# Performance work log

Measured on AMD Instinct MI355X. Metric: run time of the kernel, lower is better.

The kernel has to match this reference:

```python
import jax, jax.numpy as jnp
import numpy as np

B, S, N, C, D = 1, 6, 10000, 128, 4
HEADS, PTS = 4, 8
HF, WF = 28, 50
M = HF * WF


def setup_inputs() -> dict:
    key0 = jax.random.key(0)
    ks = jax.random.split(key0, 14)
    sc = C ** -0.5
    d = {}
    d["query"] = jax.random.normal(ks[0], (B, N, C), jnp.float32)
    d["key"] = jax.random.normal(ks[1], (S, M, B, C), jnp.float32)
    d["value"] = jax.random.normal(ks[2], (S, M, B, C), jnp.float32)
    d["query_pos"] = jax.random.normal(ks[3], (B, N, C), jnp.float32) * 0.1
    d["reference_points_cam"] = jax.random.uniform(ks[4], (S, B, N, D, 2), jnp.float32, -0.2, 1.2)
    d["bev_mask"] = jax.random.randint(ks[5], (S, B, N, D), 0, 2).astype(bool)
    d["w_off"] = jax.random.normal(ks[6], (C, HEADS * PTS * 2), jnp.float32) * sc
    d["b_off"] = jax.random.normal(ks[7], (HEADS * PTS * 2,), jnp.float32) * 0.01
    d["w_attn"] = jax.random.normal(ks[8], (C, HEADS * PTS), jnp.float32) * sc
    d["b_attn"] = jax.random.normal(ks[9], (HEADS * PTS,), jnp.float32) * 0.01
    d["w_val"] = jax.random.normal(ks[10], (C, C), jnp.float32) * sc
    d["b_val"] = jax.random.normal(ks[11], (C,), jnp.float32) * 0.01
    d["w_out"] = jax.random.normal(ks[12], (C, C), jnp.float32) * sc
    d["b_out"] = jax.random.normal(ks[13], (C,), jnp.float32) * 0.01
    d["Hf"] = HF
    d["Wf"] = WF
    return d


def reference(query, key, value, query_pos, reference_points_cam, bev_mask,
              w_off, b_off, w_attn, b_attn, w_val, b_val, w_out, b_out, Hf, Wf):
    # SpatialCrossAttention with MSDeformAttn3D (BEVFormer semantics, eval mode: dropout=identity).
    # The torch data-dependent gather/rebatch/scatter is replaced by mathematically equivalent
    # masked computation: deformable attention is per-query independent, so running it for all
    # BEV queries per camera and mask-accumulating yields identical slots.
    B_, N_, C_ = query.shape
    S_ = key.shape[0]
    D_ = reference_points_cam.shape[3]
    H, P = HEADS, PTS
    dh = C_ // H
    Pd = P // D_
    q = query + query_pos  # (B,N,C)
    off = (q @ w_off + b_off).reshape(B_, N_, H, Pd, D_, 2)
    aw = jax.nn.softmax((q @ w_attn + b_attn).reshape(B_, N_, H, P), axis=-1)  # over levels*points (L=1)
    # value projection; per-camera feature maps laid out as (B,S,H,Hf*Wf,dh)
    v = jnp.transpose(value, (2, 0, 1, 3))  # (B,S,M,C)
    v = v @ w_val + b_val
    v = v.reshape(B_, S_, Hf * Wf, H, dh).transpose(0, 1, 3, 2, 4)  # (B,S,H,M,dh)
    ref = jnp.transpose(reference_points_cam, (1, 0, 2, 3, 4))  # (B,S,N,D,2)
    norm = jnp.array([Wf, Hf], jnp.float32)  # offset_normalizer = (W, H)
    loc = ref[:, :, :, None, None, :, :] + off[:, None] / norm  # (B,S,N,H,Pd,D,2)
    loc = loc.reshape(B_, S_, N_, H, P, 2)
    # bilinear sampling, zero padding, align_corners=False
    ix = loc[..., 0] * Wf - 0.5
    iy = loc[..., 1] * Hf - 0.5
    x0 = jnp.floor(ix)
    y0 = jnp.floor(iy)

    def flat(a):  # (B,S,N,H,P) -> (B,S,H,N*P)
        return a.transpose(0, 1, 3, 2, 4).reshape(B_, S_, H, N_ * P)

    def gather(xi, yi):
        ok = (xi >= 0) & (xi < Wf) & (yi >= 0) & (yi < Hf)
        xi_c = jnp.clip(xi, 0, Wf - 1).astype(jnp.int32)
        yi_c = jnp.clip(yi, 0, Hf - 1).astype(jnp.int32)
        idx = flat(yi_c * Wf + xi_c)
        g = jnp.take_along_axis(v, idx[..., None], axis=3)  # (B,S,H,N*P,dh)
        return g * flat(ok.astype(v.dtype))[..., None]

    wx1 = ix - x0
    wy1 = iy - y0
    wx0 = 1.0 - wx1
    wy0 = 1.0 - wy1
    samp = (gather(x0, y0) * flat(wx0 * wy0)[..., None]
            + gather(x0 + 1, y0) * flat(wx1 * wy0)[..., None]
            + gather(x0, y0 + 1) * flat(wx0 * wy1)[..., None]
            + gather(x0 + 1, y0 + 1) * flat(wx1 * wy1)[..., None])  # (B,S,H,N*P,dh)
    samp = samp.reshape(B_, S_, H, N_, P, dh)
    out = jnp.einsum('bshnpd,bnhp->bsnhd', samp, aw).reshape(B_, S_, N_, C_)
    # masked scatter-accumulate back to BEV slots
    mask = jnp.transpose(jnp.any(bev_mask, axis=-1), (1, 0, 2))  # (B,S,N)
    slots = jnp.sum(out * mask[..., None].astype(out.dtype), axis=1)  # (B,N,C)
    count = jnp.maximum(mask.astype(out.dtype).sum(axis=1), 1.0)
    slots = slots / count[..., None]
    return slots @ w_out + b_out + query  # dropout is identity in eval
```

## Files before the change

kernel.cpp:

```cpp
#include <hip/hip_runtime.h>
#include <math.h>

#define S_ 6
#define N_ 10000
#define C_ 128
#define D_ 4
#define H_ 4
#define P_ 8
#define HF_ 28
#define WF_ 50
#define M_ (HF_ * WF_)
#define DH_ 32
#define SM_ (S_ * M_)

#define NB_V ((SM_ + 31) / 32)
#define NB_O ((N_ + 31) / 32)

typedef _Float16 half4v __attribute__((ext_vector_type(4)));

template <int NC, int MT, int MODE>
__device__ __forceinline__ void gemm_body(
    const float* __restrict__ A, const float* __restrict__ A2,
    const float* __restrict__ B0, const float* __restrict__ B1,
    const float* __restrict__ bias0, const float* __restrict__ bias1,
    float* __restrict__ outf, _Float16* __restrict__ outh,
    int Mrows, int m0, int tid, int nthreads, float (*Alds)[132]) {
  constexpr int NTHR = (NC / 4) * (MT / 4);

  for (int i = tid; i < MT * 32; i += nthreads) {
    int r = i >> 5, k = (i & 31) * 4;
    int row = m0 + r;
    float4 v = make_float4(0.f, 0.f, 0.f, 0.f);
    if (row < Mrows) {
      v = *(const float4*)(A + (size_t)row * C_ + k);
      if (MODE == 1) {
        float4 v2 = *(const float4*)(A2 + (size_t)row * C_ + k);
        v.x += v2.x; v.y += v2.y; v.z += v2.z; v.w += v2.w;
      }
    }
    *(float4*)(&Alds[r][k]) = v;
  }
  __syncthreads();
  if (tid >= NTHR) return;

  int ci = tid % (NC / 4);
  int mi = tid / (NC / 4);
  int c0 = ci * 4, r0 = mi * 4;

  const float* bs;
  if (MODE == 1) bs = (c0 < 64) ? bias0 + c0 : bias1 + (c0 - 64);
  else bs = bias0 + c0;

  float acc[4][4];
#pragma unroll
  for (int j = 0; j < 4; ++j)
#pragma unroll
    for (int cc = 0; cc < 4; ++cc) acc[j][cc] = bs[cc];

#pragma unroll 2
  for (int k4 = 0; k4 < C_; k4 += 4) {
    float bf[16];
#pragma unroll
    for (int kk = 0; kk < 4; ++kk) {
      int k = k4 + kk;
      float4 b4;
      if (MODE == 1)
        b4 = (c0 < 64) ? *(const float4*)(B0 + (size_t)k * 64 + c0)
                       : *(const float4*)(B1 + (size_t)k * 32 + (c0 - 64));
      else
        b4 = *(const float4*)(B0 + (size_t)k * NC + c0);
      bf[kk * 4 + 0] = b4.x; bf[kk * 4 + 1] = b4.y;
      bf[kk * 4 + 2] = b4.z; bf[kk * 4 + 3] = b4.w;
    }
    float af[16];
#pragma unroll
    for (int j = 0; j < 4; ++j) {
      float4 a4 = *(const float4*)(&Alds[r0 + j][k4]);
      af[j * 4 + 0] = a4.x; af[j * 4 + 1] = a4.y;
      af[j * 4 + 2] = a4.z; af[j * 4 + 3] = a4.w;
    }
#pragma unroll
    for (int j = 0; j < 4; ++j)
#pragma unroll
      for (int kk = 0; kk < 4; ++kk)
#pragma unroll
        for (int cc = 0; cc < 4; ++cc)
          acc[j][cc] = fmaf(af[j * 4 + kk], bf[kk * 4 + cc], acc[j][cc]);
  }

#pragma unroll
  for (int j = 0; j < 4; ++j) {
    int row = m0 + r0 + j;
    if (row >= Mrows) continue;
    if (MODE == 0) {
      int s = row / M_, mm = row % M_;
      int h = c0 >> 5, d0 = c0 & 31;
      half4v hv = {(_Float16)acc[j][0], (_Float16)acc[j][1],
                   (_Float16)acc[j][2], (_Float16)acc[j][3]};
      *(half4v*)(outh + (((size_t)s * H_ + h) * M_ + mm) * DH_ + d0) = hv;
    } else if (MODE == 1) {
      *(float4*)(outf + (size_t)row * 96 + c0) =
          make_float4(acc[j][0], acc[j][1], acc[j][2], acc[j][3]);
    } else {
      float4 qv = *(const float4*)(A2 + (size_t)row * C_ + c0);
      *(float4*)(outf + (size_t)row * C_ + c0) =
          make_float4(acc[j][0] + qv.x, acc[j][1] + qv.y,
                      acc[j][2] + qv.z, acc[j][3] + qv.w);
    }
  }
}

__global__ __launch_bounds__(256) void prep_kernel(
    const float* __restrict__ value, const float* __restrict__ w_val,
    const float* __restrict__ b_val, _Float16* __restrict__ vh,
    const float* __restrict__ query, const float* __restrict__ query_pos,
    const float* __restrict__ w_off, const float* __restrict__ b_off,
    const float* __restrict__ w_attn, const float* __restrict__ b_attn,
    float* __restrict__ OFFL) {
  __shared__ float Alds[32][132];
  int bid = blockIdx.x;
  if (bid < NB_V) {
    gemm_body<128, 32, 0>(value, nullptr, w_val, nullptr, b_val, nullptr,
                          nullptr, vh, SM_, bid * 32, threadIdx.x, 256, Alds);
  } else {
    gemm_body<96, 32, 1>(query, query_pos, w_off, w_attn, b_off, b_attn,
                         OFFL, nullptr, N_, (bid - NB_V) * 32, threadIdx.x,
                         256, Alds);
  }
}

__global__ __launch_bounds__(128) void out_kernel(
    const float* __restrict__ slots, const float* __restrict__ query,
    const float* __restrict__ w_out, const float* __restrict__ b_out,
    float* __restrict__ out) {
  __shared__ float Alds[16][132];
  gemm_body<128, 16, 2>(slots, query, w_out, nullptr, b_out, nullptr,
                        out, nullptr, N_, blockIdx.x * 16, threadIdx.x, 128,
                        Alds);
}

__global__ __launch_bounds__(128) void attn2_kernel(
    const float* __restrict__ OFFL,
    const float* __restrict__ refpts,
    const int*   __restrict__ bev_mask,
    const _Float16* __restrict__ vh,
    float* __restrict__ slots) {
  int n = blockIdx.x;
  int tid = threadIdx.x;

  __shared__ float off[64];
  __shared__ float logits[32];
  __shared__ float aw[32];
  __shared__ float refl[48];
  __shared__ int smask[6];
  __shared__ int4 sidx[192];
  __shared__ float4 sw[192];

  if (tid < 96) {
    float v = OFFL[(size_t)n * 96 + tid];
    if (tid < 64) off[tid] = v; else logits[tid - 64] = v;
  }
  if (tid < 48) {
    int s = tid >> 3, rem = tid & 7;
    refl[tid] = refpts[((size_t)s * N_ + n) * 8 + rem];
  }
  if (tid < 6) {
    const int* bm = bev_mask + ((size_t)tid * N_ + n) * D_;
    smask[tid] = (bm[0] | bm[1] | bm[2] | bm[3]) ? 1 : 0;
  }
  __syncthreads();

  if (tid < 32) {
    int h = tid >> 3;
    float mx = -1e30f;
#pragma unroll
    for (int p = 0; p < P_; ++p) mx = fmaxf(mx, logits[h * P_ + p]);
    float sum = 0.f;
#pragma unroll
    for (int p = 0; p < P_; ++p) sum += expf(logits[h * P_ + p] - mx);
    aw[tid] = expf(logits[tid] - mx) / sum;
  }
  __syncthreads();

  for (int j = tid; j < 192; j += 128) {
    int s = j >> 5, h = (j >> 3) & 3, p = j & 7;
    int pd = p >> 2, dd = p & 3;
    float rx = refl[s * 8 + dd * 2 + 0];
    float ry = refl[s * 8 + dd * 2 + 1];
    float ox = off[h * 16 + pd * 8 + dd * 2 + 0];
    float oy = off[h * 16 + pd * 8 + dd * 2 + 1];
    float ix = rx * (float)WF_ + ox - 0.5f;
    float iy = ry * (float)HF_ + oy - 0.5f;
    float x0f = floorf(ix), y0f = floorf(iy);
    int x0 = (int)x0f, y0 = (int)y0f;
    float wx1 = ix - x0f, wy1 = iy - y0f;
    float wx0 = 1.f - wx1, wy0 = 1.f - wy1;
    float a = aw[h * P_ + p];
    bool vx0 = (x0 >= 0) && (x0 < WF_);
    bool vx1 = (x0 + 1 >= 0) && (x0 + 1 < WF_);
    bool vy0 = (y0 >= 0) && (y0 < HF_);
    bool vy1 = (y0 + 1 >= 0) && (y0 + 1 < HF_);
    int x0c = min(max(x0, 0), WF_ - 1);
    int x1c = min(max(x0 + 1, 0), WF_ - 1);
    int y0c = min(max(y0, 0), HF_ - 1);
    int y1c = min(max(y0 + 1, 0), HF_ - 1);
    int base = (s * H_ + h) * M_;
    int i00 = ((base + y0c * WF_ + x0c) * DH_) * 2;
    int i10 = ((base + y0c * WF_ + x1c) * DH_) * 2;
    int i01 = ((base + y1c * WF_ + x0c) * DH_) * 2;
    int i11 = ((base + y1c * WF_ + x1c) * DH_) * 2;
    float w00 = (vx0 && vy0) ? wx0 * wy0 * a : 0.f;
    float w10 = (vx1 && vy0) ? wx1 * wy0 * a : 0.f;
    float w01 = (vx0 && vy1) ? wx0 * wy1 * a : 0.f;
    float w11 = (vx1 && vy1) ? wx1 * wy1 * a : 0.f;
    if (!(vx0 && vy0)) i00 = 0;
    if (!(vx1 && vy0)) i10 = 0;
    if (!(vx0 && vy1)) i01 = 0;
    if (!(vx1 && vy1)) i11 = 0;
    sidx[j] = make_int4(i00, i10, i01, i11);
    sw[j] = make_float4(w00, w10, w01, w11);
  }
  __syncthreads();

  int h = tid >> 5, d = tid & 31;
  int dby = d * 2;
  const char* vb = (const char*)vh;
  float acc = 0.f;
  for (int s = 0; s < S_; ++s) {
    if (!smask[s]) continue;
#pragma unroll
    for (int p = 0; p < P_; ++p) {
      int j = s * 32 + h * 8 + p;
      int4 I = sidx[j];
      float4 W = sw[j];
      float f0 = (float)*(const _Float16*)(vb + (I.x + dby));
      float f1 = (float)*(const _Float16*)(vb + (I.y + dby));
      float f2 = (float)*(const _Float16*)(vb + (I.z + dby));
      float f3 = (float)*(const _Float16*)(vb + (I.w + dby));
      acc = fmaf(f0, W.x, acc);
      acc = fmaf(f1, W.y, acc);
      acc = fmaf(f2, W.z, acc);
      acc = fmaf(f3, W.w, acc);
    }
  }
  int cnt = smask[0] + smask[1] + smask[2] + smask[3] + smask[4] + smask[5];
  float cdiv = cnt > 0 ? (float)cnt : 1.f;
  slots[(size_t)n * C_ + tid] = acc / cdiv;
}

extern "C" void kernel_launch(void* const* d_in, const int* in_sizes, int n_in,
                              void* d_out, int out_size, void* d_ws, size_t ws_size,
                              hipStream_t stream) {
  const float* query     = (const float*)d_in[0];
  const float* value     = (const float*)d_in[2];
  const float* query_pos = (const float*)d_in[3];
  const float* refpts    = (const float*)d_in[4];
  const int*   bev_mask  = (const int*)d_in[5];
  const float* w_off     = (const float*)d_in[6];
  const float* b_off     = (const float*)d_in[7];
  const float* w_attn    = (const float*)d_in[8];
  const float* b_attn    = (const float*)d_in[9];
  const float* w_val     = (const float*)d_in[10];
  const float* b_val     = (const float*)d_in[11];
  const float* w_out     = (const float*)d_in[12];
  const float* b_out     = (const float*)d_in[13];

  char* ws = (char*)d_ws;
  _Float16* vh = (_Float16*)(ws);
  float* OFFL  = (float*)(ws + 2150400);
  float* slots = (float*)(ws + 5990400);

  prep_kernel<<<NB_V + NB_O, 256, 0, stream>>>(
      value, w_val, b_val, vh, query, query_pos, w_off, b_off, w_attn, b_attn,
      OFFL);
  attn2_kernel<<<N_, 128, 0, stream>>>(OFFL, refpts, bev_mask, vh, slots);
  out_kernel<<<(N_ + 15) / 16, 128, 0, stream>>>(
      slots, query, w_out, b_out, (float*)d_out);
}
```

Baseline: 168.7 us.

## Batch four queries per attention block with vectorized half4 gathers

The attention kernel now handles four BEV queries per 128-thread block. Each thread gathers 4 contiguous fp16 channels per corner with one 8-byte load, where before it made four scalar 2-byte loads per corner, and stores the result as float4. Bilinear-times-attention weights are kept as fp16 in shared memory to save LDS space, at some cost in precision. The output GEMM is also parameterized to use 256 threads, each computing 2 rows instead of 4, to raise occupancy.

```diff
diff --git a/kernel.cpp b/kernel.cpp
--- a/kernel.cpp
+++ b/kernel.cpp
@@ -12,20 +12,21 @@
 #define M_ (HF_ * WF_)
 #define DH_ 32
 #define SM_ (S_ * M_)
+#define QB_ 4
 
 #define NB_V ((SM_ + 31) / 32)
 #define NB_O ((N_ + 31) / 32)
 
 typedef _Float16 half4v __attribute__((ext_vector_type(4)));
 
-template <int NC, int MT, int MODE>
+template <int NC, int MT, int MR, int MODE>
 __device__ __forceinline__ void gemm_body(
     const float* __restrict__ A, const float* __restrict__ A2,
     const float* __restrict__ B0, const float* __restrict__ B1,
     const float* __restrict__ bias0, const float* __restrict__ bias1,
     float* __restrict__ outf, _Float16* __restrict__ outh,
     int Mrows, int m0, int tid, int nthreads, float (*Alds)[132]) {
-  constexpr int NTHR = (NC / 4) * (MT / 4);
+  constexpr int NTHR = (NC / 4) * (MT / MR);
 
   for (int i = tid; i < MT * 32; i += nthreads) {
     int r = i >> 5, k = (i & 31) * 4;
@@ -45,15 +46,15 @@
 
   int ci = tid % (NC / 4);
   int mi = tid / (NC / 4);
-  int c0 = ci * 4, r0 = mi * 4;
+  int c0 = ci * 4, r0 = mi * MR;
 
   const float* bs;
   if (MODE == 1) bs = (c0 < 64) ? bias0 + c0 : bias1 + (c0 - 64);
   else bs = bias0 + c0;
 
-  float acc[4][4];
-#pragma unroll
-  for (int j = 0; j < 4; ++j)
+  float acc[MR][4];
+#pragma unroll
+  for (int j = 0; j < MR; ++j)
 #pragma unroll
     for (int cc = 0; cc < 4; ++cc) acc[j][cc] = bs[cc];
 
@@ -72,15 +73,15 @@
       bf[kk * 4 + 0] = b4.x; bf[kk * 4 + 1] = b4.y;
       bf[kk * 4 + 2] = b4.z; bf[kk * 4 + 3] = b4.w;
     }
-    float af[16];
-#pragma unroll
-    for (int j = 0; j < 4; ++j) {
+    float af[MR * 4];
+#pragma unroll
+    for (int j = 0; j < MR; ++j) {
       float4 a4 = *(const float4*)(&Alds[r0 + j][k4]);
       af[j * 4 + 0] = a4.x; af[j * 4 + 1] = a4.y;
       af[j * 4 + 2] = a4.z; af[j * 4 + 3] = a4.w;
     }
 #pragma unroll
-    for (int j = 0; j < 4; ++j)
+    for (int j = 0; j < MR; ++j)
 #pragma unroll
       for (int kk = 0; kk < 4; ++kk)
 #pragma unroll
@@ -89,7 +90,7 @@
   }
 
 #pragma unroll
-  for (int j = 0; j < 4; ++j) {
+  for (int j = 0; j < MR; ++j) {
     int row = m0 + r0 + j;
     if (row >= Mrows) continue;
     if (MODE == 0) {
@@ -120,23 +121,24 @@
   __shared__ float Alds[32][132];
   int bid = blockIdx.x;
   if (bid < NB_V) {
-    gemm_body<128, 32, 0>(value, nullptr, w_val, nullptr, b_val, nullptr,
-                          nullptr, vh, SM_, bid * 32, threadIdx.x, 256, Alds);
+    gemm_body<128, 32, 4, 0>(value, nullptr, w_val, nullptr, b_val, nullptr,
+                             nullptr, vh, SM_, bid * 32, threadIdx.x, 256,
+                             Alds);
   } else {
-    gemm_body<96, 32, 1>(query, query_pos, w_off, w_attn, b_off, b_attn,
-                         OFFL, nullptr, N_, (bid - NB_V) * 32, threadIdx.x,
-                         256, Alds);
-  }
-}
-
-__global__ __launch_bounds__(128) void out_kernel(
+    gemm_body<96, 32, 4, 1>(query, query_pos, w_off, w_attn, b_off, b_attn,
+                            OFFL, nullptr, N_, (bid - NB_V) * 32, threadIdx.x,
+                            256, Alds);
+  }
+}
+
+__global__ __launch_bounds__(256) void out_kernel(
     const float* __restrict__ slots, const float* __restrict__ query,
     const float* __restrict__ w_out, const float* __restrict__ b_out,
     float* __restrict__ out) {
   __shared__ float Alds[16][132];
-  gemm_body<128, 16, 2>(slots, query, w_out, nullptr, b_out, nullptr,
-                        out, nullptr, N_, blockIdx.x * 16, threadIdx.x, 128,
-                        Alds);
+  gemm_body<128, 16, 2, 2>(slots, query, w_out, nullptr, b_out, nullptr,
+                           out, nullptr, N_, blockIdx.x * 16, threadIdx.x,
+                           256, Alds);
 }
 
 __global__ __launch_bounds__(128) void attn2_kernel(
@@ -145,57 +147,61 @@
     const int*   __restrict__ bev_mask,
     const _Float16* __restrict__ vh,
     float* __restrict__ slots) {
-  int n = blockIdx.x;
+  int n0 = blockIdx.x * QB_;
   int tid = threadIdx.x;
 
-  __shared__ float off[64];
-  __shared__ float logits[32];
-  __shared__ float aw[32];
-  __shared__ float refl[48];
-  __shared__ int smask[6];
-  __shared__ int4 sidx[192];
-  __shared__ float4 sw[192];
-
-  if (tid < 96) {
-    float v = OFFL[(size_t)n * 96 + tid];
-    if (tid < 64) off[tid] = v; else logits[tid - 64] = v;
-  }
-  if (tid < 48) {
-    int s = tid >> 3, rem = tid & 7;
-    refl[tid] = refpts[((size_t)s * N_ + n) * 8 + rem];
-  }
-  if (tid < 6) {
-    const int* bm = bev_mask + ((size_t)tid * N_ + n) * D_;
-    smask[tid] = (bm[0] | bm[1] | bm[2] | bm[3]) ? 1 : 0;
+  __shared__ float off[QB_][64];
+  __shared__ float logits[QB_][32];
+  __shared__ float aw[QB_][32];
+  __shared__ float refl[QB_][48];
+  __shared__ int smask[QB_][6];
+  __shared__ int4 sidx[QB_][194];
+  __shared__ half4v swh[QB_][194];
+
+  for (int i = tid; i < QB_ * 96; i += 128) {
+    int q = i / 96, c = i % 96;
+    float v = OFFL[(size_t)(n0 + q) * 96 + c];
+    if (c < 64) off[q][c] = v; else logits[q][c - 64] = v;
+  }
+  for (int i = tid; i < QB_ * 48; i += 128) {
+    int q = i / 48, rem = i % 48;
+    int s = rem >> 3, r8 = rem & 7;
+    refl[q][rem] = refpts[((size_t)s * N_ + (n0 + q)) * 8 + r8];
+  }
+  if (tid < QB_ * 6) {
+    int q = tid / 6, s = tid % 6;
+    const int* bm = bev_mask + ((size_t)s * N_ + (n0 + q)) * D_;
+    smask[q][s] = (bm[0] | bm[1] | bm[2] | bm[3]) ? 1 : 0;
   }
   __syncthreads();
 
-  if (tid < 32) {
-    int h = tid >> 3;
+  {
+    int q = tid >> 5, j = tid & 31, h = j >> 3;
     float mx = -1e30f;
 #pragma unroll
-    for (int p = 0; p < P_; ++p) mx = fmaxf(mx, logits[h * P_ + p]);
+    for (int p = 0; p < P_; ++p) mx = fmaxf(mx, logits[q][h * P_ + p]);
     float sum = 0.f;
 #pragma unroll
-    for (int p = 0; p < P_; ++p) sum += expf(logits[h * P_ + p] - mx);
-    aw[tid] = expf(logits[tid] - mx) / sum;
+    for (int p = 0; p < P_; ++p) sum += expf(logits[q][h * P_ + p] - mx);
+    aw[q][j] = expf(logits[q][j] - mx) / sum;
   }
   __syncthreads();
 
-  for (int j = tid; j < 192; j += 128) {
-    int s = j >> 5, h = (j >> 3) & 3, p = j & 7;
+  for (int i = tid; i < QB_ * 192; i += 128) {
+    int q = i / 192, j = i % 192;
+    int s = j >> 5, w32 = j & 31, p = w32 >> 2, h = w32 & 3;
     int pd = p >> 2, dd = p & 3;
-    float rx = refl[s * 8 + dd * 2 + 0];
-    float ry = refl[s * 8 + dd * 2 + 1];
-    float ox = off[h * 16 + pd * 8 + dd * 2 + 0];
-    float oy = off[h * 16 + pd * 8 + dd * 2 + 1];
+    float rx = refl[q][s * 8 + dd * 2 + 0];
+    float ry = refl[q][s * 8 + dd * 2 + 1];
+    float ox = off[q][h * 16 + pd * 8 + dd * 2 + 0];
+    float oy = off[q][h * 16 + pd * 8 + dd * 2 + 1];
     float ix = rx * (float)WF_ + ox - 0.5f;
     float iy = ry * (float)HF_ + oy - 0.5f;
     float x0f = floorf(ix), y0f = floorf(iy);
     int x0 = (int)x0f, y0 = (int)y0f;
     float wx1 = ix - x0f, wy1 = iy - y0f;
     float wx0 = 1.f - wx1, wy0 = 1.f - wy1;
-    float a = aw[h * P_ + p];
+    float a = aw[q][h * P_ + p];
     bool vx0 = (x0 >= 0) && (x0 < WF_);
     bool vx1 = (x0 + 1 >= 0) && (x0 + 1 < WF_);
     bool vy0 = (y0 >= 0) && (y0 < HF_);
@@ -217,35 +223,51 @@
     if (!(vx1 && vy0)) i10 = 0;
     if (!(vx0 && vy1)) i01 = 0;
     if (!(vx1 && vy1)) i11 = 0;
-    sidx[j] = make_int4(i00, i10, i01, i11);
-    sw[j] = make_float4(w00, w10, w01, w11);
+    sidx[q][j] = make_int4(i00, i10, i01, i11);
+    half4v wv = {(_Float16)w00, (_Float16)w10, (_Float16)w01, (_Float16)w11};
+    swh[q][j] = wv;
   }
   __syncthreads();
 
-  int h = tid >> 5, d = tid & 31;
-  int dby = d * 2;
-  const char* vb = (const char*)vh;
-  float acc = 0.f;
+  int q = tid >> 5, t = tid & 31, h = t >> 3, c8 = t & 7;
+  const char* vbase = (const char*)vh + c8 * 8;
+  float acc0 = 0.f, acc1 = 0.f, acc2 = 0.f, acc3 = 0.f;
   for (int s = 0; s < S_; ++s) {
-    if (!smask[s]) continue;
+    if (!smask[q][s]) continue;
 #pragma unroll
     for (int p = 0; p < P_; ++p) {
-      int j = s * 32 + h * 8 + p;
-      int4 I = sidx[j];
-      float4 W = sw[j];
-      float f0 = (float)*(const _Float16*)(vb + (I.x + dby));
-      float f1 = (float)*(const _Float16*)(vb + (I.y + dby));
-      float f2 = (float)*(const _Float16*)(vb + (I.z + dby));
-      float f3 = (float)*(const _Float16*)(vb + (I.w + dby));
-      acc = fmaf(f0, W.x, acc);
-      acc = fmaf(f1, W.y, acc);
-      acc = fmaf(f2, W.z, acc);
-      acc = fmaf(f3, W.w, acc);
-    }
-  }
-  int cnt = smask[0] + smask[1] + smask[2] + smask[3] + smask[4] + smask[5];
-  float cdiv = cnt > 0 ? (float)cnt : 1.f;
-  slots[(size_t)n * C_ + tid] = acc / cdiv;
+      int j = s * 32 + p * 4 + h;
+      int4 I = sidx[q][j];
+      half4v W = swh[q][j];
+      half4v a4 = *(const half4v*)(vbase + I.x);
+      half4v b4 = *(const half4v*)(vbase + I.y);
+      half4v c4 = *(const half4v*)(vbase + I.z);
+      half4v d4 = *(const half4v*)(vbase + I.w);
+      float w0 = (float)W[0], w1 = (float)W[1];
+      float w2 = (float)W[2], w3 = (float)W[3];
+      acc0 = fmaf((float)a4[0], w0, acc0);
+      acc1 = fmaf((float)a4[1], w0, acc1);
+      acc2 = fmaf((float)a4[2], w0, acc2);
+      acc3 = fmaf((float)a4[3], w0, acc3);
+      acc0 = fmaf((float)b4[0], w1, acc0);
+      acc1 = fmaf((float)b4[1], w1, acc1);
+      acc2 = fmaf((float)b4[2], w1, acc2);
+      acc3 = fmaf((float)b4[3], w1, acc3);
+      acc0 = fmaf((float)c4[0], w2, acc0);
+      acc1 = fmaf((float)c4[1], w2, acc1);
+      acc2 = fmaf((float)c4[2], w2, acc2);
+      acc3 = fmaf((float)c4[3], w2, acc3);
+      acc0 = fmaf((float)d4[0], w3, acc0);
+      acc1 = fmaf((float)d4[1], w3, acc1);
+      acc2 = fmaf((float)d4[2], w3, acc2);
+      acc3 = fmaf((float)d4[3], w3, acc3);
+    }
+  }
+  int cnt = smask[q][0] + smask[q][1] + smask[q][2] +
+            smask[q][3] + smask[q][4] + smask[q][5];
+  float inv = 1.f / (float)(cnt > 0 ? cnt : 1);
+  float4 r = make_float4(acc0 * inv, acc1 * inv, acc2 * inv, acc3 * inv);
+  *(float4*)(slots + (size_t)(n0 + q) * C_ + h * DH_ + c8 * 4) = r;
 }
 
 extern "C" void kernel_launch(void* const* d_in, const int* in_sizes, int n_in,
@@ -273,7 +295,8 @@
   prep_kernel<<<NB_V + NB_O, 256, 0, stream>>>(
       value, w_val, b_val, vh, query, query_pos, w_off, b_off, w_attn, b_attn,
       OFFL);
-  attn2_kernel<<<N_, 128, 0, stream>>>(OFFL, refpts, bev_mask, vh, slots);
-  out_kernel<<<(N_ + 15) / 16, 128, 0, stream>>>(
+  attn2_kernel<<<N_ / QB_, 128, 0, stream>>>(OFFL, refpts, bev_mask, vh,
+                                             slots);
+  out_kernel<<<(N_ + 15) / 16, 256, 0, stream>>>(
       slots, query, w_out, b_out, (float*)d_out);
 }
```

After: 165.6 us. No clear change (-1.8%).
